# Optimization experiments

Measured on AMD Instinct MI355X. Metric: run time of the kernel, lower is better.

The kernel has to match this reference:

```python
import jax, jax.numpy as jnp
import numpy as np

P = 16      # patch size
D = 768     # d_model
H = 12      # heads
L = 12      # layers
F = 3072    # d_ff
NC = 1000   # num classes
B = 32
IMG = 224
S = (IMG // P) ** 2 + 1  # 197 tokens (CLS + patches)
EPS = 1e-5


def layernorm(x, s, b):
    m = jnp.mean(x, axis=-1, keepdims=True)
    v = jnp.var(x, axis=-1, keepdims=True)
    return (x - m) * jax.lax.rsqrt(v + EPS) * s + b


def setup_inputs() -> dict:
    key = jax.random.key(0)
    ks = jax.random.split(key, 16)
    sd = 0.02
    patch_dim = P * P * 3  # 768
    inp = {
        "img": jax.random.normal(ks[0], (B, 3, IMG, IMG), jnp.float32),
        "proj_w": jax.random.normal(ks[1], (patch_dim, D), jnp.float32) * sd,
        "proj_b": jnp.zeros((D,), jnp.float32),
        "cls_token": jax.random.normal(ks[2], (1, 1, D), jnp.float32) * sd,
        "pos_emb": jax.random.normal(ks[3], (1, S, D), jnp.float32) * sd,
        # stacked per-layer params [L, ...]
        "ln1_s": jnp.ones((L, D), jnp.float32),
        "ln1_b": jnp.zeros((L, D), jnp.float32),
        "wq": jax.random.normal(ks[4], (L, D, D), jnp.float32) * sd,
        "bq": jnp.zeros((L, D), jnp.float32),
        "wk": jax.random.normal(ks[5], (L, D, D), jnp.float32) * sd,
        "bk": jnp.zeros((L, D), jnp.float32),
        "wv": jax.random.normal(ks[6], (L, D, D), jnp.float32) * sd,
        "bv": jnp.zeros((L, D), jnp.float32),
        "wo": jax.random.normal(ks[7], (L, D, D), jnp.float32) * sd,
        "bo": jnp.zeros((L, D), jnp.float32),
        "ln2_s": jnp.ones((L, D), jnp.float32),
        "ln2_b": jnp.zeros((L, D), jnp.float32),
        "w1": jax.random.normal(ks[8], (L, D, F), jnp.float32) * sd,
        "b1": jnp.zeros((L, F), jnp.float32),
        "w2": jax.random.normal(ks[9], (L, F, D), jnp.float32) * sd,
        "b2": jnp.zeros((L, D), jnp.float32),
        "fnorm_s": jnp.ones((D,), jnp.float32),
        "fnorm_b": jnp.zeros((D,), jnp.float32),
        "head_w": jax.random.normal(ks[10], (D, NC), jnp.float32) * sd,
        "head_b": jnp.zeros((NC,), jnp.float32),
    }
    return inp


def vit_forward(img, proj_w, proj_b, cls_token, pos_emb, ln1_s, ln1_b,
                wq, bq, wk, bk, wv, bv, wo, bo, ln2_s, ln2_b,
                w1, b1, w2, b2, fnorm_s, fnorm_b, head_w, head_b):
    b = img.shape[0]
    g = IMG // P
    # rearrange 'b c (h ph) (w pw) -> b (h w) (ph pw c)'
    x = img.reshape(b, 3, g, P, g, P)
    x = x.transpose(0, 2, 4, 3, 5, 1).reshape(b, g * g, P * P * 3)
    x = x @ proj_w + proj_b                      # [b, 196, D]
    cls = jnp.broadcast_to(cls_token, (b, 1, D))
    x = jnp.concatenate([cls, x], axis=1)        # [b, 197, D]
    x = x + pos_emb                              # learnable positional encoding

    dk = D // H
    scale = 1.0 / jnp.sqrt(jnp.float32(dk))

    def layer(x, p):
        (l1s, l1b, Wq, Bq, Wk, Bk, Wv, Bv, Wo, Bo,
         l2s, l2b, W1, B1, W2, B2) = p
        # pre-norm self-attention with residual
        xn = layernorm(x, l1s, l1b)
        q = (xn @ Wq + Bq).reshape(b, S, H, dk)
        k = (xn @ Wk + Bk).reshape(b, S, H, dk)
        v = (xn @ Wv + Bv).reshape(b, S, H, dk)
        scores = jnp.einsum('bqhd,bkhd->bhqk', q, k) * scale
        attn = jax.nn.softmax(scores, axis=-1)
        ao = jnp.einsum('bhqk,bkhd->bqhd', attn, v).reshape(b, S, D)
        x = x + (ao @ Wo + Bo)
        # pre-norm FFN with residual
        xn = layernorm(x, l2s, l2b)
        h = jax.nn.gelu(xn @ W1 + B1, approximate=False)
        x = x + (h @ W2 + B2)
        return x, None

    params = (ln1_s, ln1_b, wq, bq, wk, bk, wv, bv, wo, bo,
              ln2_s, ln2_b, w1, b1, w2, b2)
    x, _ = jax.lax.scan(layer, x, params)
    x = layernorm(x, fnorm_s, fnorm_b)
    cls_out = x[:, 0, :]
    return cls_out @ head_w + head_b             # [b, num_classes]


def reference(img, proj_w, proj_b, cls_token, pos_emb, ln1_s, ln1_b,
              wq, bq, wk, bk, wv, bv, wo, bo, ln2_s, ln2_b,
              w1, b1, w2, b2, fnorm_s, fnorm_b, head_w, head_b):
    return vit_forward(img, proj_w, proj_b, cls_token, pos_emb, ln1_s, ln1_b,
                       wq, bq, wk, bk, wv, bv, wo, bo, ln2_s, ln2_b,
                       w1, b1, w2, b2, fnorm_s, fnorm_b, head_w, head_b)
```

## Files before the change

kernel.cpp:

```cpp
#include <hip/hip_runtime.h>
#include <stdint.h>

typedef __attribute__((ext_vector_type(4))) float  f32x4;
typedef __attribute__((ext_vector_type(8))) _Float16 f16x8;
typedef __attribute__((ext_vector_type(8))) unsigned short u16x8;

__device__ __forceinline__ unsigned short f2h(float f) {
    _Float16 h = (_Float16)f;
    union { _Float16 h; unsigned short u; } cv; cv.h = h; return cv.u;
}

__device__ __forceinline__ f32x4 mfma16(f16x8 a, f16x8 b, f32x4 c) {
    return __builtin_amdgcn_mfma_f32_16x16x32_f16(a, b, c, 0, 0, 0);
}

__device__ __forceinline__ void async16(const unsigned short* g, unsigned short* l) {
    __builtin_amdgcn_global_load_lds(
        (const __attribute__((address_space(1))) unsigned int*)g,
        (__attribute__((address_space(3))) unsigned int*)l,
        16, 0, 0);
}

template<int EPI, int BK>
__global__ __launch_bounds__(256, (BK == 32 ? 4 : 3))
void gemm_k(const unsigned short* __restrict__ A, const unsigned short* __restrict__ Bw,
            int M, int K, int N,
            float* __restrict__ p0, unsigned short* __restrict__ p1,
            const float* __restrict__ p2, const float* __restrict__ p3,
            unsigned short* __restrict__ p4, unsigned short* __restrict__ p5)
{
    constexpr int SMSTG = 2 * 64 * BK + 2 * 128 * BK;
    constexpr int SMU   = (EPI == 0 || EPI == 2)
                          ? (SMSTG > 64 * 136 ? SMSTG : 64 * 136)
                          : SMSTG;
    __shared__ unsigned short smem[SMU];
    unsigned short (*lA)[64 * BK]  = (unsigned short(*)[64 * BK])smem;
    unsigned short (*lB)[128 * BK] = (unsigned short(*)[128 * BK])(smem + 2 * 64 * BK);
    const int tid  = threadIdx.x;
    const int lane = tid & 63;
    const int wid  = tid >> 6;

    const int gx  = gridDim.x;
    const int nwg = gx * gridDim.y;
    const int lin = blockIdx.y * gx + blockIdx.x;
    const int q = nwg >> 3, r = nwg & 7;
    const int xcd = lin & 7, i = lin >> 3;
    const int wg  = (xcd < r ? xcd * (q + 1) : r * (q + 1) + (xcd - r) * q) + i;
    const int m0 = (wg / gx) * 64;
    const int n0 = (wg % gx) * 128;

    const int colBase = wid * 32;
    const int fr = lane & 15, fg = lane >> 4;

    f32x4 acc[4][2];
#pragma unroll
    for (int a = 0; a < 4; ++a)
#pragma unroll
        for (int b = 0; b < 2; ++b) acc[a][b] = (f32x4){0.f, 0.f, 0.f, 0.f};

    const int nk = K / BK;
    constexpr int CPR = BK / 8;
    constexpr int ACH = 64 * CPR;
    constexpr int NH  = (ACH + 128 * CPR) / 256;

    auto stage = [&](int buf, int kt) {
        const int k0 = kt * BK;
#pragma unroll
        for (int h = 0; h < NH; ++h) {
            const int c = h * 256 + tid;
            const int wbase = h * 256 + wid * 64;
            if (c < ACH) {
                const int row = c / CPR, kc = c % CPR;
                const int gkc = (BK == 32) ? (kc ^ ((row >> 1) & 3)) : (kc ^ (row & 7));
                int ar = m0 + row; if (ar > M - 1) ar = M - 1;
                async16(A + (size_t)ar * K + k0 + gkc * 8,
                        &lA[buf][(size_t)wbase * 8]);
            } else {
                const int cb = c - ACH;
                const int row = cb / CPR, kc = cb % CPR;
                const int gkc = (BK == 32) ? (kc ^ ((row >> 1) & 3)) : (kc ^ (row & 7));
                async16(Bw + (size_t)(n0 + row) * K + k0 + gkc * 8,
                        &lB[buf][(size_t)(wbase - ACH) * 8]);
            }
        }
    };

    stage(0, 0);
    for (int kt = 0; kt < nk; ++kt) {
        __syncthreads();
        if (kt + 1 < nk) stage((kt + 1) & 1, kt + 1);
        const int buf = kt & 1;
#pragma unroll
        for (int kk = 0; kk < BK / 32; ++kk) {
            f16x8 af[4], bfv[2];
#pragma unroll
            for (int mi = 0; mi < 4; ++mi) {
                int row = mi * 16 + fr;
                int pc  = (BK == 32) ? (fg ^ ((row >> 1) & 3))
                                     : ((kk * 4 + fg) ^ (row & 7));
                af[mi] = *(const f16x8*)(&lA[buf][row * BK + pc * 8]);
            }
#pragma unroll
            for (int ni = 0; ni < 2; ++ni) {
                int row = colBase + ni * 16 + fr;
                int pc  = (BK == 32) ? (fg ^ ((row >> 1) & 3))
                                     : ((kk * 4 + fg) ^ (row & 7));
                bfv[ni] = *(const f16x8*)(&lB[buf][row * BK + pc * 8]);
            }
#pragma unroll
            for (int mi = 0; mi < 4; ++mi)
#pragma unroll
                for (int ni = 0; ni < 2; ++ni)
                    acc[mi][ni] = mfma16(af[mi], bfv[ni], acc[mi][ni]);
        }
    }

    const int mat0 = (EPI == 0) ? (n0 / 768) : 0;

    if constexpr (EPI == 0 || EPI == 2) {
        if (EPI == 2 || mat0 < 2) {
            unsigned short* sm = smem;
            __syncthreads();
#pragma unroll
            for (int mi = 0; mi < 4; ++mi)
#pragma unroll
                for (int ni = 0; ni < 2; ++ni) {
                    const int lcol = colBase + ni * 16 + fr;
                    const int colg = n0 + lcol;
#pragma unroll
                    for (int reg = 0; reg < 4; ++reg) {
                        const int lrow = mi * 16 + fg * 4 + reg;
                        float val = acc[mi][ni][reg] + p2[colg];
                        if (EPI == 2)
                            val = 0.5f * val * (1.0f + erff(val * 0.70710678118654752f));
                        sm[lrow * 136 + lcol] = f2h(val);
                    }
                }
            __syncthreads();
#pragma unroll
            for (int it = 0; it < 4; ++it) {
                const int e = it * 256 + tid;
                const int lrow = e >> 4, cch = e & 15;
                const int grow = m0 + lrow;
                if (grow >= M) continue;
                const u16x8 v = *(const u16x8*)(&sm[lrow * 136 + cch * 8]);
                if (EPI == 2) {
                    *(u16x8*)(p1 + (size_t)grow * 3072 + n0 + cch * 8) = v;
                } else {
                    const int colg = n0 + cch * 8;
                    const int w = colg - mat0 * 768;
                    const int h = w >> 6, d = w & 63;
                    const int b = grow / 197, s = grow - b * 197;
                    unsigned short* dst = (mat0 == 0) ? p1 : p4;
                    *(u16x8*)(dst + ((((size_t)b * 12 + h) * 197 + s) * 64 + d)) = v;
                }
            }
        } else {
#pragma unroll
            for (int mi = 0; mi < 4; ++mi)
#pragma unroll
                for (int ni = 0; ni < 2; ++ni) {
                    const int col = n0 + colBase + ni * 16 + fr;
                    const int w = col - 1536;
                    const int h = w >> 6, d = w & 63;
#pragma unroll
                    for (int reg = 0; reg < 4; ++reg) {
                        const int row = m0 + mi * 16 + fg * 4 + reg;
                        if (row >= M) continue;
                        const int b = row / 197, s = row - b * 197;
                        float val = acc[mi][ni][reg] + p2[col];
                        p5[(((size_t)b * 12 + h) * 64 + d) * 208 + s] = f2h(val);
                    }
                }
        }
    } else {
#pragma unroll
        for (int mi = 0; mi < 4; ++mi) {
#pragma unroll
            for (int ni = 0; ni < 2; ++ni) {
                const int col = n0 + colBase + ni * 16 + fr;
#pragma unroll
                for (int reg = 0; reg < 4; ++reg) {
                    const int row = m0 + mi * 16 + fg * 4 + reg;
                    if (row >= M) continue;
                    const float v = acc[mi][ni][reg];
                    if constexpr (EPI == 1 || EPI == 3) {
                        size_t idx = (size_t)row * 768 + col;
                        p0[idx] = p0[idx] + v + p2[col];
                    } else {
                        int b = row / 196, p = row - b * 196;
                        float val = v + p2[col] + p3[(size_t)(1 + p) * 768 + col];
                        p0[((size_t)(b * 197 + 1 + p)) * 768 + col] = val;
                    }
                }
            }
        }
    }
}

__device__ __forceinline__ void convT_body(const float* __restrict__ src,
                                           unsigned short* __restrict__ dst,
                                           int K, int N, int bx, int by,
                                           float (*t)[65])
{
    const int tid = threadIdx.x;
    const int n0 = bx * 64, k0 = by * 64;
    int r = tid >> 4, cq = tid & 15;
#pragma unroll
    for (int i = 0; i < 4; ++i) {
        f32x4 v = *(const f32x4*)(src + (size_t)(k0 + r + i * 16) * N + n0 + cq * 4);
        t[r + i * 16][cq * 4 + 0] = v.x;
        t[r + i * 16][cq * 4 + 1] = v.y;
        t[r + i * 16][cq * 4 + 2] = v.z;
        t[r + i * 16][cq * 4 + 3] = v.w;
    }
    __syncthreads();
    int nl = tid >> 2, kq = tid & 3;
    u16x8 o0, o1;
#pragma unroll
    for (int j = 0; j < 8; ++j) {
        o0[j] = f2h(t[kq * 16 + j][nl]);
        o1[j] = f2h(t[kq * 16 + 8 + j][nl]);
    }
    unsigned short* d = dst + (size_t)(n0 + nl) * K + k0 + kq * 16;
    *(u16x8*)(d)     = o0;
    *(u16x8*)(d + 8) = o1;
}

__device__ __forceinline__ void prep_block(int pid,
            const float* __restrict__ wq, const float* __restrict__ wk,
            const float* __restrict__ wv, const float* __restrict__ wo,
            const float* __restrict__ w1, const float* __restrict__ w2,
            const float* __restrict__ bq, const float* __restrict__ bk,
            const float* __restrict__ bv,
            unsigned short* __restrict__ wqkvT, unsigned short* __restrict__ woT,
            unsigned short* __restrict__ w1T, unsigned short* __restrict__ w2T,
            float* __restrict__ bqkv, float (*t)[65])
{
    if (pid == 1728) {
        for (int c = threadIdx.x; c < 2304; c += 256) {
            int m = c / 768, w = c - m * 768;
            bqkv[c] = (m == 0) ? bq[w] : (m == 1 ? bk[w] : bv[w]);
        }
        return;
    }
    const float* src; unsigned short* dst; int K, N, bx, by;
    if (pid < 576) {
        int mat = pid / 144, r = pid - mat * 144;
        K = 768; N = 768; bx = r % 12; by = r / 12;
        if (mat == 0)      { src = wq; dst = wqkvT; }
        else if (mat == 1) { src = wk; dst = wqkvT + 768ull * 768; }
        else if (mat == 2) { src = wv; dst = wqkvT + 1536ull * 768; }
        else               { src = wo; dst = woT; }
    } else if (pid < 1152) {
        int r = pid - 576; K = 768; N = 3072; bx = r % 48; by = r / 48;
        src = w1; dst = w1T;
    } else {
        int r = pid - 1152; K = 3072; N = 768; bx = r % 12; by = r / 12;
        src = w2; dst = w2T;
    }
    convT_body(src, dst, K, N, bx, by, t);
}

__global__ __launch_bounds__(256)
void prep_k(const float* __restrict__ wq, const float* __restrict__ wk,
            const float* __restrict__ wv, const float* __restrict__ wo,
            const float* __restrict__ w1, const float* __restrict__ w2,
            const float* __restrict__ bq, const float* __restrict__ bk,
            const float* __restrict__ bv,
            unsigned short* __restrict__ wqkvT, unsigned short* __restrict__ woT,
            unsigned short* __restrict__ w1T, unsigned short* __restrict__ w2T,
            float* __restrict__ bqkv)
{
    __shared__ float t[64][65];
    prep_block(blockIdx.x, wq, wk, wv, wo, w1, w2, bq, bk, bv,
               wqkvT, woT, w1T, w2T, bqkv, t);
}

__global__ __launch_bounds__(256, 4)
void attn_prep_k(const unsigned short* __restrict__ qb, const unsigned short* __restrict__ kb,
                 const unsigned short* __restrict__ vt, unsigned short* __restrict__ ao,
                 const float* __restrict__ wq, const float* __restrict__ wk,
                 const float* __restrict__ wv, const float* __restrict__ wo,
                 const float* __restrict__ w1, const float* __restrict__ w2,
                 const float* __restrict__ bq, const float* __restrict__ bk,
                 const float* __restrict__ bv,
                 unsigned short* __restrict__ wqkvT, unsigned short* __restrict__ woT,
                 unsigned short* __restrict__ w1T, unsigned short* __restrict__ w2T,
                 float* __restrict__ bqkv)
{
    __shared__ float smbuf[32 * 210 + 32];

    const int bid = blockIdx.x;
    if (bid >= 2688) {
        prep_block(bid - 2688, wq, wk, wv, wo, w1, w2, bq, bk, bv,
                   wqkvT, woT, w1T, w2T, bqkv,
                   reinterpret_cast<float(*)[65]>(smbuf));
        return;
    }

    float* sc   = smbuf;
    float* rinv = smbuf + 32 * 210;

    const int bh = bid % 384;
    const int qt = bid / 384;
    const int b = bh / 12, h = bh - b * 12;
    const unsigned short* qh  = qb + (size_t)bh * 197 * 64;
    const unsigned short* kh  = kb + (size_t)bh * 197 * 64;
    const unsigned short* vth = vt + (size_t)bh * 64 * 208;
    const int tid = threadIdx.x, lane = tid & 63, wid = tid >> 6;
    const int fr = lane & 15, fg = lane >> 4;

    f16x8 qf[2][2];
#pragma unroll
    for (int mi = 0; mi < 2; ++mi)
#pragma unroll
        for (int kc = 0; kc < 2; ++kc) {
            int s = qt * 32 + mi * 16 + fr; if (s > 196) s = 196;
            qf[mi][kc] = *(const f16x8*)(qh + (size_t)s * 64 + kc * 32 + fg * 8);
        }

    for (int nt = wid; nt < 13; nt += 4) {
        f32x4 a0 = (f32x4){0.f,0.f,0.f,0.f}, a1 = a0;
        int rs = nt * 16 + fr; if (rs > 196) rs = 196;
#pragma unroll
        for (int kc = 0; kc < 2; ++kc) {
            f16x8 kf = *(const f16x8*)(kh + (size_t)rs * 64 + kc * 32 + fg * 8);
            a0 = mfma16(qf[0][kc], kf, a0);
            a1 = mfma16(qf[1][kc], kf, a1);
        }
        int ccol = nt * 16 + fr;
        bool valid = (ccol < 197);
#pragma unroll
        for (int reg = 0; reg < 4; ++reg) {
            int mr = fg * 4 + reg;
            sc[mr * 210 + ccol]        = valid ? a0[reg] * 0.125f : -1e30f;
            sc[(16 + mr) * 210 + ccol] = valid ? a1[reg] * 0.125f : -1e30f;
        }
    }
    __syncthreads();

    {
        int row = tid >> 3, j = tid & 7;
        float m = -1e30f;
        for (int c = j; c < 208; c += 8) m = fmaxf(m, sc[row * 210 + c]);
#pragma unroll
        for (int o = 1; o < 8; o <<= 1) m = fmaxf(m, __shfl_xor(m, o));
        float sum = 0.f;
        for (int c = j; c < 208; c += 8) {
            float e = __expf(sc[row * 210 + c] - m);
            sc[row * 210 + c] = e;
            sum += e;
        }
#pragma unroll
        for (int o = 1; o < 8; o <<= 1) sum += __shfl_xor(sum, o);
        if (j == 0) rinv[row] = 1.0f / sum;
    }
    __syncthreads();

    f32x4 o0 = (f32x4){0.f,0.f,0.f,0.f}, o1 = o0;
    const int dbase = wid * 16;
    for (int kt = 0; kt < 7; ++kt) {
        int kb8 = kt * 32 + fg * 8;
        f16x8 pa0, pa1, vf;
        if (kb8 >= 208) {
#pragma unroll
            for (int j = 0; j < 8; ++j) { pa0[j] = (_Float16)0.f; pa1[j] = (_Float16)0.f; vf[j] = (_Float16)0.f; }
        } else {
            const float* pr0 = &sc[fr * 210 + kb8];
            const float* pr1 = &sc[(16 + fr) * 210 + kb8];
#pragma unroll
            for (int j = 0; j < 8; ++j) { pa0[j] = (_Float16)pr0[j]; pa1[j] = (_Float16)pr1[j]; }
            vf = *(const f16x8*)(vth + (size_t)(dbase + fr) * 208 + kb8);
        }
        o0 = mfma16(pa0, vf, o0);
        o1 = mfma16(pa1, vf, o1);
    }
#pragma unroll
    for (int reg = 0; reg < 4; ++reg) {
        int mr0 = fg * 4 + reg, s0 = qt * 32 + mr0;
        if (s0 < 197)
            ao[((size_t)(b * 197 + s0)) * 768 + h * 64 + dbase + fr] = f2h(o0[reg] * rinv[mr0]);
        int mr1 = 16 + fg * 4 + reg, s1 = qt * 32 + mr1;
        if (s1 < 197)
            ao[((size_t)(b * 197 + s1)) * 768 + h * 64 + dbase + fr] = f2h(o1[reg] * rinv[mr1]);
    }
}

__global__ __launch_bounds__(256, 4)
void ln_k(const float* __restrict__ x, const float* __restrict__ gs,
          const float* __restrict__ gb, unsigned short* __restrict__ out)
{
    const int row = blockIdx.x;
    const int tid = threadIdx.x, lane = tid & 63, wid = tid >> 6;
    const float* xr = x + (size_t)row * 768;
    float v0 = xr[tid], v1 = xr[tid + 256], v2 = xr[tid + 512];
    float s = v0 + v1 + v2;
    float q = v0 * v0 + v1 * v1 + v2 * v2;
#pragma unroll
    for (int o = 1; o < 64; o <<= 1) { s += __shfl_xor(s, o); q += __shfl_xor(q, o); }
    __shared__ float ws[4], wq[4];
    if (lane == 0) { ws[wid] = s; wq[wid] = q; }
    __syncthreads();
    s = ws[0] + ws[1] + ws[2] + ws[3];
    q = wq[0] + wq[1] + wq[2] + wq[3];
    const float mean = s * (1.0f / 768.0f);
    const float rstd = rsqrtf(q * (1.0f / 768.0f) - mean * mean + 1e-5f);
    unsigned short* orow = out + (size_t)row * 768;
    orow[tid]       = f2h((v0 - mean) * rstd * gs[tid]       + gb[tid]);
    orow[tid + 256] = f2h((v1 - mean) * rstd * gs[tid + 256] + gb[tid + 256]);
    orow[tid + 512] = f2h((v2 - mean) * rstd * gs[tid + 512] + gb[tid + 512]);
}

__global__ __launch_bounds__(256)
void convT_k(const float* __restrict__ src, unsigned short* __restrict__ dst, int K, int N)
{
    __shared__ float t[64][65];
    convT_body(src, dst, K, N, blockIdx.x, blockIdx.y, t);
}

__global__ __launch_bounds__(256)
void patch_k(const float* __restrict__ img, unsigned short* __restrict__ patches)
{
    const int t = blockIdx.x;
    const int pxy = threadIdx.x;
    const int b = t / 196, pi = t - b * 196;
    const int gy = pi / 14, gx = pi - gy * 14;
    const int py = pxy >> 4, px = pxy & 15;
    const int yy = gy * 16 + py, xx = gx * 16 + px;
    const float* base = img + ((size_t)b * 3 * 224 + yy) * 224 + xx;
    float c0 = base[0];
    float c1 = base[224 * 224];
    float c2 = base[2 * 224 * 224];
    unsigned short* d = patches + (size_t)t * 768 + pxy * 3;
    d[0] = f2h(c0); d[1] = f2h(c1); d[2] = f2h(c2);
}

__global__ void cls_k(const float* __restrict__ cls, const float* __restrict__ pos,
                      float* __restrict__ x)
{
    int c = blockIdx.x * 256 + threadIdx.x;
    int b = blockIdx.y;
    x[((size_t)b * 197) * 768 + c] = cls[c] + pos[c];
}

__global__ __launch_bounds__(256, 4)
void head_k(const float* __restrict__ x, const float* __restrict__ fs, const float* __restrict__ fb,
            const float* __restrict__ hw, const float* __restrict__ hb, float* __restrict__ out)
{
    __shared__ float xn[768];
    __shared__ float ws[4], wq_[4];
    const int b  = blockIdx.y;
    const int n0 = blockIdx.x * 125;
    const int tid = threadIdx.x, lane = tid & 63, wid = tid >> 6;
    const float* xr = x + (size_t)b * 197 * 768;
    float v0 = xr[tid], v1 = xr[tid + 256], v2 = xr[tid + 512];
    float s = v0 + v1 + v2, q = v0 * v0 + v1 * v1 + v2 * v2;
#pragma unroll
    for (int o = 1; o < 64; o <<= 1) { s += __shfl_xor(s, o); q += __shfl_xor(q, o); }
    if (lane == 0) { ws[wid] = s; wq_[wid] = q; }
    __syncthreads();
    s = ws[0] + ws[1] + ws[2] + ws[3];
    q = wq_[0] + wq_[1] + wq_[2] + wq_[3];
    float mean = s * (1.f / 768.f);
    float rstd = rsqrtf(q * (1.f / 768.f) - mean * mean + 1e-5f);
    xn[tid]       = (v0 - mean) * rstd * fs[tid]       + fb[tid];
    xn[tid + 256] = (v1 - mean) * rstd * fs[tid + 256] + fb[tid + 256];
    xn[tid + 512] = (v2 - mean) * rstd * fs[tid + 512] + fb[tid + 512];
    __syncthreads();

    const int nrel = tid >> 1, half = tid & 1;
    const int n = n0 + nrel;
    float acc = 0.f;
    if (nrel < 125) {
        const float* hp = hw + (size_t)(half * 384) * 1000 + n;
        const float* xp = xn + half * 384;
#pragma unroll 4
        for (int k = 0; k < 384; ++k) acc = fmaf(xp[k], hp[(size_t)k * 1000], acc);
    }
    acc += __shfl_xor(acc, 1);
    if (half == 0 && nrel < 125) out[(size_t)b * 1000 + n] = acc + hb[n];
}

extern "C" void kernel_launch(void* const* d_in, const int* in_sizes, int n_in,
                              void* d_out, int out_size, void* d_ws, size_t ws_size,
                              hipStream_t stream)
{
    (void)in_sizes; (void)n_in; (void)out_size; (void)ws_size;
    const float* img    = (const float*)d_in[0];
    const float* proj_w = (const float*)d_in[1];
    const float* proj_b = (const float*)d_in[2];
    const float* cls_t  = (const float*)d_in[3];
    const float* pos    = (const float*)d_in[4];
    const float* ln1_s  = (const float*)d_in[5];
    const float* ln1_b  = (const float*)d_in[6];
    const float* wq     = (const float*)d_in[7];
    const float* bq     = (const float*)d_in[8];
    const float* wk     = (const float*)d_in[9];
    const float* bk     = (const float*)d_in[10];
    const float* wv     = (const float*)d_in[11];
    const float* bv     = (const float*)d_in[12];
    const float* wo     = (const float*)d_in[13];
    const float* bo     = (const float*)d_in[14];
    const float* ln2_s  = (const float*)d_in[15];
    const float* ln2_b  = (const float*)d_in[16];
    const float* w1     = (const float*)d_in[17];
    const float* b1     = (const float*)d_in[18];
    const float* w2     = (const float*)d_in[19];
    const float* b2     = (const float*)d_in[20];
    const float* fs     = (const float*)d_in[21];
    const float* fb     = (const float*)d_in[22];
    const float* hw     = (const float*)d_in[23];
    const float* hb     = (const float*)d_in[24];

    char* ws = (char*)d_ws;
    size_t off = 0;
    auto alloc = [&](size_t bytes) -> char* {
        char* r = ws + off;
        off += (bytes + 255) & ~(size_t)255;
        return r;
    };
    unsigned short* wqkvT[2]; unsigned short* woT[2];
    unsigned short* w1T[2];   unsigned short* w2T[2];
    float* bqkv[2];
    for (int s = 0; s < 2; ++s) {
        wqkvT[s] = (unsigned short*)alloc(2304ull * 768 * 2);
        woT[s]   = (unsigned short*)alloc(768ull * 768 * 2);
        w1T[s]   = (unsigned short*)alloc(3072ull * 768 * 2);
        w2T[s]   = (unsigned short*)alloc(768ull * 3072 * 2);
        bqkv[s]  = (float*)alloc(2304 * 4);
    }
    unsigned short* projT = (unsigned short*)alloc(768ull * 768 * 2);
    float*          x     = (float*)alloc(6304ull * 768 * 4);
    unsigned short* xn    = (unsigned short*)alloc(6304ull * 768 * 2);
    unsigned short* qbuf  = (unsigned short*)alloc(4841472ull * 2);
    unsigned short* kbuf  = (unsigned short*)alloc(4841472ull * 2);
    unsigned short* vbufT = (unsigned short*)alloc(384ull * 64 * 208 * 2);
    unsigned short* aob   = (unsigned short*)alloc(6304ull * 768 * 2);
    unsigned short* hbuf  = (unsigned short*)alloc(6304ull * 3072 * 2);
    unsigned short* patches = hbuf;

    convT_k<<<dim3(12, 12), 256, 0, stream>>>(proj_w, projT, 768, 768);
    patch_k<<<dim3(6272), 256, 0, stream>>>(img, patches);
    prep_k<<<dim3(1729), 256, 0, stream>>>(
        wq, wk, wv, wo, w1, w2, bq, bk, bv,
        wqkvT[0], woT[0], w1T[0], w2T[0], bqkv[0]);
    gemm_k<4, 32><<<dim3(6, 98), 256, 0, stream>>>(patches, projT, 6272, 768, 768,
                                                   x, nullptr, proj_b, pos, nullptr, nullptr);
    cls_k<<<dim3(3, 32), 256, 0, stream>>>(cls_t, pos, x);

    for (int l = 0; l < 12; ++l) {
        const int set = l & 1, nxt = set ^ 1;
        const int lp  = (l < 11) ? l + 1 : 11;
        const int nprep = (l < 11) ? 1729 : 0;

        ln_k<<<dim3(6304), 256, 0, stream>>>(x, ln1_s + l * 768, ln1_b + l * 768, xn);
        gemm_k<0, 32><<<dim3(18, 99), 256, 0, stream>>>(xn, wqkvT[set], 6304, 768, 2304,
                                                        nullptr, qbuf, bqkv[set], nullptr, kbuf, vbufT);
        attn_prep_k<<<dim3(2688 + nprep), 256, 0, stream>>>(
            qbuf, kbuf, vbufT, aob,
            wq + (size_t)lp * 768 * 768, wk + (size_t)lp * 768 * 768,
            wv + (size_t)lp * 768 * 768, wo + (size_t)lp * 768 * 768,
            w1 + (size_t)lp * 768 * 3072, w2 + (size_t)lp * 3072 * 768,
            bq + lp * 768, bk + lp * 768, bv + lp * 768,
            wqkvT[nxt], woT[nxt], w1T[nxt], w2T[nxt], bqkv[nxt]);
        gemm_k<1, 32><<<dim3(6, 99), 256, 0, stream>>>(aob, woT[set], 6304, 768, 768,
                                                       x, nullptr, bo + l * 768, nullptr, nullptr, nullptr);
        ln_k<<<dim3(6304), 256, 0, stream>>>(x, ln2_s + l * 768, ln2_b + l * 768, xn);
        gemm_k<2, 32><<<dim3(24, 99), 256, 0, stream>>>(xn, w1T[set], 6304, 768, 3072,
                                                        nullptr, hbuf, b1 + l * 3072, nullptr, nullptr, nullptr);
        gemm_k<3, 64><<<dim3(6, 99), 256, 0, stream>>>(hbuf, w2T[set], 6304, 3072, 768,
                                                       x, nullptr, b2 + l * 768, nullptr, nullptr, nullptr);
    }

    head_k<<<dim3(8, 32), 256, 0, stream>>>(x, fs, fb, hw, hb, (float*)d_out);
}
```

Before: 3.034 ms.

## Fuse LayerNorm into residual GEMM epilogue via last-block atomic counter

Removes the standalone LayerNorm launches after the Wo and W2 GEMMs. Each row-tile of 64 rows counts finished column blocks with an atomic, and the last block to finish normalises those full rows and writes the fp16 normalised activations. This saves kernel launches and a separate pass over x. In exchange, one block per row tile serially does LN over 64 rows with 4 waves, which adds tail latency and relies on threadfence and atomic ordering being correct.

After: 6.254 ms. 2.06x slower.

```diff
diff --git a/kernel.cpp b/kernel.cpp
--- a/kernel.cpp
+++ b/kernel.cpp
@@ -27,7 +27,9 @@
             int M, int K, int N,
             float* __restrict__ p0, unsigned short* __restrict__ p1,
             const float* __restrict__ p2, const float* __restrict__ p3,
-            unsigned short* __restrict__ p4, unsigned short* __restrict__ p5)
+            unsigned short* __restrict__ p4, unsigned short* __restrict__ p5,
+            const float* __restrict__ lngs, const float* __restrict__ lngb,
+            unsigned short* __restrict__ xnout, int* __restrict__ cnt)
 {
     constexpr int SMSTG = 2 * 64 * BK + 2 * 128 * BK;
     constexpr int SMU   = (EPI == 0 || EPI == 2)
@@ -193,6 +195,40 @@
                         p0[((size_t)(b * 197 + 1 + p)) * 768 + col] = val;
                     }
                 }
+            }
+        }
+    }
+
+    if constexpr (EPI == 1 || EPI == 3) {
+        if (lngs != nullptr) {
+            __shared__ int lastFlag;
+            __threadfence();
+            if (tid == 0) {
+                int old = atomicAdd(&cnt[m0 >> 6], 1);
+                lastFlag = (old == (int)gridDim.x - 1) ? 1 : 0;
+            }
+            __syncthreads();
+            if (lastFlag) {
+                __threadfence();
+                for (int rr = wid; rr < 64; rr += 4) {
+                    const int row = m0 + rr;
+                    if (row >= M) continue;
+                    const float* xr = p0 + (size_t)row * 768;
+                    float s = 0.f, q2 = 0.f;
+                    for (int c = lane; c < 768; c += 64) {
+                        float v = xr[c]; s += v; q2 += v * v;
+                    }
+#pragma unroll
+                    for (int o = 1; o < 64; o <<= 1) {
+                        s += __shfl_xor(s, o); q2 += __shfl_xor(q2, o);
+                    }
+                    const float mean = s * (1.0f / 768.0f);
+                    const float rstd = rsqrtf(q2 * (1.0f / 768.0f) - mean * mean + 1e-5f);
+                    unsigned short* orow = xnout + (size_t)row * 768;
+                    for (int c = lane; c < 768; c += 64)
+                        orow[c] = f2h((xr[c] - mean) * rstd * lngs[c] + lngb[c]);
+                }
+                if (tid == 0) cnt[m0 >> 6] = 0;
             }
         }
     }
@@ -538,7 +574,10 @@
     unsigned short* vbufT = (unsigned short*)alloc(384ull * 64 * 208 * 2);
     unsigned short* aob   = (unsigned short*)alloc(6304ull * 768 * 2);
     unsigned short* hbuf  = (unsigned short*)alloc(6304ull * 3072 * 2);
+    int*            lncnt = (int*)alloc(128 * 4);
     unsigned short* patches = hbuf;
+
+    hipMemsetAsync(lncnt, 0, 128 * 4, stream);
 
     convT_k<<<dim3(12, 12), 256, 0, stream>>>(proj_w, projT, 768, 768);
     patch_k<<<dim3(6272), 256, 0, stream>>>(img, patches);
@@ -546,17 +585,20 @@
         wq, wk, wv, wo, w1, w2, bq, bk, bv,
         wqkvT[0], woT[0], w1T[0], w2T[0], bqkv[0]);
     gemm_k<4, 32><<<dim3(6, 98), 256, 0, stream>>>(patches, projT, 6272, 768, 768,
-                                                   x, nullptr, proj_b, pos, nullptr, nullptr);
+                                                   x, nullptr, proj_b, pos, nullptr, nullptr,
+                                                   nullptr, nullptr, nullptr, nullptr);
     cls_k<<<dim3(3, 32), 256, 0, stream>>>(cls_t, pos, x);
+
+    ln_k<<<dim3(6304), 256, 0, stream>>>(x, ln1_s, ln1_b, xn);
 
     for (int l = 0; l < 12; ++l) {
         const int set = l & 1, nxt = set ^ 1;
         const int lp  = (l < 11) ? l + 1 : 11;
         const int nprep = (l < 11) ? 1729 : 0;
 
-        ln_k<<<dim3(6304), 256, 0, stream>>>(x, ln1_s + l * 768, ln1_b + l * 768, xn);
         gemm_k<0, 32><<<dim3(18, 99), 256, 0, stream>>>(xn, wqkvT[set], 6304, 768, 2304,
-                                                        nullptr, qbuf, bqkv[set], nullptr, kbuf, vbufT);
+                                                        nullptr, qbuf, bqkv[set], nullptr, kbuf, vbufT,
+                                                        nullptr, nullptr, nullptr, nullptr);
         attn_prep_k<<<dim3(2688 + nprep), 256, 0, stream>>>(
             qbuf, kbuf, vbufT, aob,
             wq + (size_t)lp * 768 * 768, wk + (size_t)lp * 768 * 768,
@@ -565,12 +607,16 @@
             bq + lp * 768, bk + lp * 768, bv + lp * 768,
             wqkvT[nxt], woT[nxt], w1T[nxt], w2T[nxt], bqkv[nxt]);
         gemm_k<1, 32><<<dim3(6, 99), 256, 0, stream>>>(aob, woT[set], 6304, 768, 768,
-                                                       x, nullptr, bo + l * 768, nullptr, nullptr, nullptr);
-        ln_k<<<dim3(6304), 256, 0, stream>>>(x, ln2_s + l * 768, ln2_b + l * 768, xn);
+                                                       x, nullptr, bo + l * 768, nullptr, nullptr, nullptr,
+                                                       ln2_s + l * 768, ln2_b + l * 768, xn, lncnt);
         gemm_k<2, 32><<<dim3(24, 99), 256, 0, stream>>>(xn, w1T[set], 6304, 768, 3072,
-                                                        nullptr, hbuf, b1 + l * 3072, nullptr, nullptr, nullptr);
+                                                        nullptr, hbuf, b1 + l * 3072, nullptr, nullptr, nullptr,
+                                                        nullptr, nullptr, nullptr, nullptr);
+        const float* ngs = (l < 11) ? (ln1_s + (l + 1) * 768) : nullptr;
+        const float* ngb = (l < 11) ? (ln1_b + (l + 1) * 768) : nullptr;
         gemm_k<3, 64><<<dim3(6, 99), 256, 0, stream>>>(hbuf, w2T[set], 6304, 3072, 768,
-                                                       x, nullptr, b2 + l * 768, nullptr, nullptr, nullptr);
+                                                       x, nullptr, b2 + l * 768, nullptr, nullptr, nullptr,
+                                                       ngs, ngb, xn, lncnt);
     }
 
     head_k<<<dim3(8, 32), 256, 0, stream>>>(x, fs, fb, hw, hb, (float*)d_out);
```
